# Kernel optimization log

Hardware: AMD Instinct MI355X
Metric: run time of the kernel (lower is better)

The kernel has to match this reference:

```python
import jax, jax.numpy as jnp
import numpy as np

N, F_DIM, H_DIM = 8192, 128, 128

def setup_inputs() -> dict:
    key = jax.random.key(0)
    ks = jax.random.split(key, 7)
    inp = {
        "input": jax.random.normal(ks[0], (N, F_DIM), dtype=jnp.float32),
        "wavelets": jax.random.normal(ks[1], (N, N), dtype=jnp.float32) / np.sqrt(N),
        "wavelets_inv": jax.random.normal(ks[2], (N, N), dtype=jnp.float32) / np.sqrt(N),
        # layer 1 params
        "W1": jax.random.uniform(ks[3], (F_DIM, H_DIM), dtype=jnp.float32,
                                 minval=-np.sqrt(6.0/(F_DIM+H_DIM)), maxval=np.sqrt(6.0/(F_DIM+H_DIM))),
        "f1": jax.random.uniform(ks[4], (N,), dtype=jnp.float32, minval=0.9, maxval=1.1),
        # layer 2 params
        "W2": jax.random.uniform(ks[5], (H_DIM, H_DIM), dtype=jnp.float32,
                                 minval=-np.sqrt(6.0/(H_DIM+H_DIM)), maxval=np.sqrt(6.0/(H_DIM+H_DIM))),
        "f2": jax.random.uniform(ks[6], (N,), dtype=jnp.float32, minval=0.9, maxval=1.1),
    }
    return inp

def _gwnn_layer(features, wavelets, wavelets_inv, W, filt):
    # torch: wavelets @ diag(filt) @ (wavelets_inv @ (features @ W))
    # diag(filt) matmul == column-wise scale of wavelets (broadcast elementwise)
    xw = features @ W                      # [N, out]
    spec = wavelets_inv @ xw               # [N, out] spectral-domain features
    spec = filt[:, None] * spec            # apply learnable diagonal filter
    return wavelets @ spec                 # [N, out]

def reference(input, wavelets, wavelets_inv, W1, f1, W2, f2):
    # eval mode: dropout is identity
    h1 = jax.nn.relu(_gwnn_layer(input, wavelets, wavelets_inv, W1, f1))
    out = _gwnn_layer(h1, wavelets, wavelets_inv, W2, f2)
    return out
```

## Files before the change

### kernel.cpp

```cpp
#include <hip/hip_runtime.h>
#include <hip/hip_bf16.h>
#include <stdint.h>


typedef __attribute__((ext_vector_type(4))) float f32x4;
typedef __attribute__((ext_vector_type(8))) short s16x8;
typedef __attribute__((ext_vector_type(4))) short s16x4;

#define DEVI static __device__ __forceinline__

DEVI short bf1(float x){ __bf16 h = (__bf16)x; return __builtin_bit_cast(short, h); }

DEVI s16x8 cvt8(f32x4 lo, f32x4 hi){
  s16x8 r;
#pragma unroll
  for (int i = 0; i < 4; ++i){ r[i] = bf1(lo[i]); r[4+i] = bf1(hi[i]); }
  return r;
}

DEVI void glds16(const void* g, void* l){
  __builtin_amdgcn_global_load_lds((const __attribute__((address_space(1))) void*)g,
                                   (__attribute__((address_space(3))) void*)l, 16, 0, 0);
}

template<int N> DEVI void waitvm(){
  if constexpr (N == 0)       asm volatile("s_waitcnt vmcnt(0)"  ::: "memory");
  else if constexpr (N == 5)  asm volatile("s_waitcnt vmcnt(5)"  ::: "memory");
  else if constexpr (N == 6)  asm volatile("s_waitcnt vmcnt(6)"  ::: "memory");
  else if constexpr (N == 12) asm volatile("s_waitcnt vmcnt(12)" ::: "memory");
}

__global__ __launch_bounds__(256, 1) void gemm_big(
    const float* __restrict__ Ap, const short* __restrict__ Btp,
    float* __restrict__ Pp, int K, int M)
{
  constexpr int BM = 128, BK = 64;
  constexpr int ASZ = BM*BK*4;
  constexpr int BSZ = 128*BK*2;
  constexpr int TSZ = ASZ + BSZ;
  constexpr int NBUF = 3, PRE = 2;
  __shared__ uint8_t lds[NBUF*TSZ];

  const int tid  = threadIdx.x;
  const int lane = tid & 63;
  const int wv   = tid >> 6;
  const int la   = lane & 15;
  const int g4   = lane >> 4;
  const int bxl  = ((blockIdx.x & 7) << 3) + (blockIdx.x >> 3);
  const int m0   = bxl * BM;
  const int kq   = blockIdx.y;
  const int K4   = K >> 2;
  const int kb   = kq * K4;

  const float* gAbase = Ap + (size_t)m0*K + kb;
  int aoffg[8];
#pragma unroll
  for (int j = 0; j < 8; ++j){
    const int rl = (wv<<5) + (j<<2) + (lane>>4);
    aoffg[j] = rl*K + (((lane&15) ^ (rl&15))<<2);
  }

  const int nb0 = (wv<<5) + (lane>>3);
  const short* gB0 = Btp + (size_t)(nb0    )*K + kb + (((lane&7)^(nb0&7))<<3);
  const short* gB1 = Btp + (size_t)(nb0+ 8 )*K + kb + (((lane&7)^(nb0&7))<<3);
  const short* gB2 = Btp + (size_t)(nb0+16 )*K + kb + (((lane&7)^(nb0&7))<<3);
  const short* gB3 = Btp + (size_t)(nb0+24 )*K + kb + (((lane&7)^(nb0&7))<<3);

  int aoff[2][2][2];
#pragma unroll
  for (int mi = 0; mi < 2; ++mi){
    const int r = (wv<<5) + mi*16 + la;
#pragma unroll
    for (int kf = 0; kf < 2; ++kf){
      const int v0 = kf*8 + (g4<<1);
      aoff[mi][kf][0] = r*256 + (((v0  )^(r&15))<<4);
      aoff[mi][kf][1] = r*256 + (((v0+1)^(r&15))<<4);
    }
  }
  int boff[8][2];
#pragma unroll
  for (int ni = 0; ni < 8; ++ni){
    const int n = ni*16 + la;
#pragma unroll
    for (int kf = 0; kf < 2; ++kf){
      const int u = kf*4 + g4;
      boff[ni][kf] = n*128 + ((u^(n&7))<<4);
    }
  }

  f32x4 acc[2][8] = {};

  int kk = 0;
  uint8_t* const lend = lds + NBUF*TSZ;
  uint8_t* bs = lds;
  uint8_t* bc = lds;

  auto STAGE = [&](){
    uint8_t* Ab = bs;
    uint8_t* Bb = bs + ASZ;
#pragma unroll
    for (int j = 0; j < 8; ++j)
      glds16(gAbase + aoffg[j] + kk, Ab + (wv<<13) + (j<<10));
    kk += BK;
    glds16(gB0, Bb + (wv<<12));
    glds16(gB1, Bb + (wv<<12) + 1024);
    glds16(gB2, Bb + (wv<<12) + 2048);
    glds16(gB3, Bb + (wv<<12) + 3072);
    gB0 += BK; gB1 += BK; gB2 += BK; gB3 += BK;
    bs += TSZ; if (bs == lend) bs = lds;
  };

  auto COMPUTE = [&](){
    const uint8_t* Ab = bc;
    const uint8_t* Bb = bc + ASZ;
#pragma unroll
    for (int kf = 0; kf < 2; ++kf){
      s16x8 a0 = cvt8(*(const f32x4*)(Ab + aoff[0][kf][0]),
                      *(const f32x4*)(Ab + aoff[0][kf][1]));
      s16x8 a1 = cvt8(*(const f32x4*)(Ab + aoff[1][kf][0]),
                      *(const f32x4*)(Ab + aoff[1][kf][1]));
#pragma unroll
      for (int ni = 0; ni < 8; ++ni){
        s16x8 b = *(const s16x8*)(Bb + boff[ni][kf]);
        acc[0][ni] = __builtin_amdgcn_mfma_f32_16x16x32_bf16(a0, b, acc[0][ni], 0, 0, 0);
        acc[1][ni] = __builtin_amdgcn_mfma_f32_16x16x32_bf16(a1, b, acc[1][ni], 0, 0, 0);
      }
    }
    bc += TSZ; if (bc == lend) bc = lds;
  };

  const int ns = K4 >> 6;
  for (int s = 0; s < PRE && s < ns; ++s) STAGE();

  for (int t = 0; t < ns; ++t){
    if (t < ns - 1) waitvm<12>();
    else            waitvm<0>();
    __builtin_amdgcn_s_barrier();
    asm volatile("" ::: "memory");
    if (t + PRE < ns) STAGE();
    COMPUTE();
    asm volatile("" ::: "memory");
  }

  float* P = Pp + (size_t)kq * M * 128;
  const int rbase = m0 + (wv<<5) + (g4<<2);
#pragma unroll
  for (int mi = 0; mi < 2; ++mi)
#pragma unroll
    for (int ni = 0; ni < 8; ++ni)
#pragma unroll
      for (int r = 0; r < 4; ++r)
        P[(size_t)(rbase + mi*16 + r)*128 + ni*16 + la] = acc[mi][ni][r];
}

template<bool ABF>
__global__ __launch_bounds__(256, 1) void sgemm(
    const void* __restrict__ Ap, const short* __restrict__ Btp,
    void* __restrict__ Outp, int K, int M)
{
  constexpr int BM = 32, BN = 128, BK = 64;
  constexpr int ASZ = ABF ? BM*BK*2 : BM*BK*4;
  constexpr int BSZ = BN*BK*2;
  constexpr int TSZ = ASZ + BSZ;
  constexpr int NL  = ABF ? 5 : 6;
  constexpr int NBUF = 3, PRE = 2;
  __shared__ uint8_t lds[NBUF*TSZ];

  const int tid  = threadIdx.x;
  const int lane = tid & 63;
  const int wv   = tid >> 6;
  const int la   = lane & 15;
  const int g4   = lane >> 4;
  const int m0   = blockIdx.x * BM;

  const float* gA0 = nullptr; const float* gA1 = nullptr; const short* gAh = nullptr;
  if constexpr (!ABF){
    const float* Af = (const float*)Ap;
    int r0 = (wv<<3) + (lane>>4);
    int r1 = r0 + 4;
    gA0 = Af + (size_t)(m0+r0)*K + (((lane&15)^(r0&15))<<2);
    gA1 = Af + (size_t)(m0+r1)*K + (((lane&15)^(r1&15))<<2);
  } else {
    const short* Ah = (const short*)Ap;
    int r = (wv<<3) + (lane>>3);
    gAh = Ah + (size_t)(m0+r)*K + (((lane&7)^(r&7))<<3);
  }
  const int nb0 = (wv<<5) + (lane>>3);
  const short* gB0 = Btp + (size_t)(nb0    )*K + (((lane&7)^(nb0&7))<<3);
  const short* gB1 = Btp + (size_t)(nb0+ 8 )*K + (((lane&7)^(nb0&7))<<3);
  const short* gB2 = Btp + (size_t)(nb0+16 )*K + (((lane&7)^(nb0&7))<<3);
  const short* gB3 = Btp + (size_t)(nb0+24 )*K + (((lane&7)^(nb0&7))<<3);

  int aoff[2][2][2];
  int boff[2][2];
#pragma unroll
  for (int mi = 0; mi < 2; ++mi){
    const int r = mi*16 + la;
#pragma unroll
    for (int kf = 0; kf < 2; ++kf){
      if constexpr (!ABF){
        const int v0 = kf*8 + (g4<<1);
        aoff[mi][kf][0] = r*256 + (((v0  )^(r&15))<<4);
        aoff[mi][kf][1] = r*256 + (((v0+1)^(r&15))<<4);
      } else {
        const int u = kf*4 + g4;
        aoff[mi][kf][0] = r*128 + ((u^(r&7))<<4);
        aoff[mi][kf][1] = 0;
      }
    }
  }
#pragma unroll
  for (int ni = 0; ni < 2; ++ni){
    const int n = (wv<<5) + ni*16 + la;
#pragma unroll
    for (int kf = 0; kf < 2; ++kf){
      const int u = kf*4 + g4;
      boff[ni][kf] = n*128 + ((u^(n&7))<<4);
    }
  }

  f32x4 acc[2][2] = {};

  auto STAGE = [&](uint8_t* buf){
    uint8_t* Ab = buf;
    uint8_t* Bb = buf + ASZ;
    if constexpr (!ABF){
      glds16(gA0, Ab + (wv<<11));
      glds16(gA1, Ab + (wv<<11) + 1024);
      gA0 += BK; gA1 += BK;
    } else {
      glds16(gAh, Ab + (wv<<10));
      gAh += BK;
    }
    glds16(gB0, Bb + (wv<<12));
    glds16(gB1, Bb + (wv<<12) + 1024);
    glds16(gB2, Bb + (wv<<12) + 2048);
    glds16(gB3, Bb + (wv<<12) + 3072);
    gB0 += BK; gB1 += BK; gB2 += BK; gB3 += BK;
  };

  auto COMPUTE = [&](const uint8_t* buf){
    const uint8_t* Ab = buf;
    const uint8_t* Bb = buf + ASZ;
#pragma unroll
    for (int kf = 0; kf < 2; ++kf){
      s16x8 a0, a1, b0, b1;
      if constexpr (!ABF){
        a0 = cvt8(*(const f32x4*)(Ab + aoff[0][kf][0]), *(const f32x4*)(Ab + aoff[0][kf][1]));
        a1 = cvt8(*(const f32x4*)(Ab + aoff[1][kf][0]), *(const f32x4*)(Ab + aoff[1][kf][1]));
      } else {
        a0 = *(const s16x8*)(Ab + aoff[0][kf][0]);
        a1 = *(const s16x8*)(Ab + aoff[1][kf][0]);
      }
      b0 = *(const s16x8*)(Bb + boff[0][kf]);
      b1 = *(const s16x8*)(Bb + boff[1][kf]);
      acc[0][0] = __builtin_amdgcn_mfma_f32_16x16x32_bf16(a0, b0, acc[0][0], 0, 0, 0);
      acc[0][1] = __builtin_amdgcn_mfma_f32_16x16x32_bf16(a0, b1, acc[0][1], 0, 0, 0);
      acc[1][0] = __builtin_amdgcn_mfma_f32_16x16x32_bf16(a1, b0, acc[1][0], 0, 0, 0);
      acc[1][1] = __builtin_amdgcn_mfma_f32_16x16x32_bf16(a1, b1, acc[1][1], 0, 0, 0);
    }
  };

  const int ns = K >> 6;
  uint8_t* const lend = lds + NBUF*TSZ;
  uint8_t* bs = lds;
  uint8_t* bc = lds;
  for (int s = 0; s < PRE && s < ns; ++s){
    STAGE(bs);
    bs += TSZ; if (bs == lend) bs = lds;
  }
  for (int t = 0; t < ns; ++t){
    if (t < ns - 1) waitvm<NL>(); else waitvm<0>();
    __builtin_amdgcn_s_barrier();
    asm volatile("" ::: "memory");
    if (t + PRE < ns){
      STAGE(bs);
      bs += TSZ; if (bs == lend) bs = lds;
    }
    COMPUTE(bc);
    bc += TSZ; if (bc == lend) bc = lds;
    asm volatile("" ::: "memory");
  }

  const int mbase = m0 + (g4<<2);
  const int nc0   = (wv<<5) + la;
#pragma unroll
  for (int mi = 0; mi < 2; ++mi){
#pragma unroll
    for (int ni = 0; ni < 2; ++ni){
      s16x4 pk;
#pragma unroll
      for (int r = 0; r < 4; ++r) pk[r] = bf1(acc[mi][ni][r]);
      *(s16x4*)((short*)Outp + (size_t)(nc0 + (ni<<4))*M + (mbase + (mi<<4))) = pk;
    }
  }
}


__global__ __launch_bounds__(256) void red_t(
    const float* __restrict__ Pp, const float* __restrict__ fp,
    short* __restrict__ out, int M)
{
  __shared__ short t[128*65];
  const size_t S = (size_t)M*128;
  const int m0 = blockIdx.x * 64;
  const int tid = threadIdx.x;
#pragma unroll
  for (int it = 0; it < 8; ++it){
    const int idx = it*256 + tid;
    const int m = idx >> 5, nq = idx & 31;
    const float* base = Pp + (size_t)(m0+m)*128;
    f32x4 a = ((const f32x4*)(base      ))[nq];
    f32x4 b = ((const f32x4*)(base +   S))[nq];
    f32x4 c = ((const f32x4*)(base + 2*S))[nq];
    f32x4 d = ((const f32x4*)(base + 3*S))[nq];
    const float fv = fp[m0+m];
#pragma unroll
    for (int j = 0; j < 4; ++j)
      t[(nq*4+j)*65 + m] = bf1(fv * ((a[j] + b[j]) + (c[j] + d[j])));
  }
  __syncthreads();
#pragma unroll
  for (int it = 0; it < 8; ++it){
    const int idx = it*256 + tid;
    const int n = idx >> 4, mc = idx & 15;
    s16x4 v;
#pragma unroll
    for (int j = 0; j < 4; ++j) v[j] = t[n*65 + mc*4 + j];
    *(s16x4*)(out + (size_t)n*M + m0 + mc*4) = v;
  }
}

__global__ __launch_bounds__(256) void red_r(
    const float* __restrict__ Pp, short* __restrict__ out, int M)
{
  const size_t S = (size_t)M*128;
  const size_t i0 = (size_t)(blockIdx.x*256 + threadIdx.x) * 8;
  s16x8 v;
#pragma unroll
  for (int h = 0; h < 2; ++h){
    f32x4 a = *(const f32x4*)(Pp + i0 + 4*h);
    f32x4 b = *(const f32x4*)(Pp + i0 + 4*h + S);
    f32x4 c = *(const f32x4*)(Pp + i0 + 4*h + 2*S);
    f32x4 d = *(const f32x4*)(Pp + i0 + 4*h + 3*S);
#pragma unroll
    for (int j = 0; j < 4; ++j)
      v[4*h+j] = bf1(fmaxf((a[j] + b[j]) + (c[j] + d[j]), 0.0f));
  }
  *(s16x8*)(out + i0) = v;
}

__global__ __launch_bounds__(256) void red_f(
    const float* __restrict__ Pp, float* __restrict__ out, int M)
{
  const size_t S = (size_t)M*128;
  const size_t i0 = (size_t)(blockIdx.x*256 + threadIdx.x) * 4;
  f32x4 a = *(const f32x4*)(Pp + i0);
  f32x4 b = *(const f32x4*)(Pp + i0 + S);
  f32x4 c = *(const f32x4*)(Pp + i0 + 2*S);
  f32x4 d = *(const f32x4*)(Pp + i0 + 3*S);
  *(f32x4*)(out + i0) = (a + b) + (c + d);
}

__global__ void wtrans_k(const float* __restrict__ W1, const float* __restrict__ W2,
                         short* __restrict__ T1, short* __restrict__ T2){
  const int idx = blockIdx.x*256 + threadIdx.x;
  const int m = idx >> 14, rem = idx & 16383;
  const int n = rem >> 7, k = rem & 127;
  const float* W = m ? W2 : W1;
  short* T = m ? T2 : T1;
  T[n*128 + k] = bf1(W[k*128 + n]);
}

extern "C" void kernel_launch(void* const* d_in, const int* in_sizes, int n_in,
                              void* d_out, int out_size, void* d_ws, size_t ws_size,
                              hipStream_t stream){
  const float* input = (const float*)d_in[0];
  const float* wav   = (const float*)d_in[1];
  const float* winv  = (const float*)d_in[2];
  const float* W1    = (const float*)d_in[3];
  const float* f1    = (const float*)d_in[4];
  const float* W2    = (const float*)d_in[5];
  const float* f2    = (const float*)d_in[6];

  constexpr int M = 8192;
  uint8_t* ws = (uint8_t*)d_ws;
  short* W1T = (short*)(ws);
  short* W2T = (short*)(ws + (32<<10));
  short* XWT = (short*)(ws + (64<<10));
  short* SPT = (short*)(ws + (64<<10) + (2<<20));
  short* H1  = (short*)(ws + (64<<10) + (4<<20));
  float* P   = (float*)(ws + (64<<10) + (6<<20));

  dim3 b(256);
  dim3 gbig(M/128, 4);
  dim3 gns(M/32);
  dim3 grt(M/64);
  dim3 grr(M*128/(256*8));
  dim3 grf(M*128/(256*4));
  dim3 gt(128);

  wtrans_k<<<gt, b, 0, stream>>>(W1, W2, W1T, W2T);
  sgemm<false><<<gns, b, 0, stream>>>(input, W1T, XWT, 128, M);
  gemm_big<<<gbig, b, 0, stream>>>(winv, XWT, P, M, M);
  red_t  <<<grt, b, 0, stream>>>(P, f1, SPT, M);
  gemm_big<<<gbig, b, 0, stream>>>(wav, SPT, P, M, M);
  red_r  <<<grr, b, 0, stream>>>(P, H1, M);
  sgemm<true ><<<gns, b, 0, stream>>>(H1, W2T, XWT, 128, M);
  gemm_big<<<gbig, b, 0, stream>>>(winv, XWT, P, M, M);
  red_t  <<<grt, b, 0, stream>>>(P, f2, SPT, M);
  gemm_big<<<gbig, b, 0, stream>>>(wav, SPT, P, M, M);
  red_f  <<<grf, b, 0, stream>>>(P, (float*)d_out, M);
}
```

Measured before the change: 290.2 us.

## Halve K-tile and deepen LDS pipeline to four stages in flight

Shrinks the K tile of the big split-K GEMM from 64 to 32 and raises the ring from 3 to 6 LDS buffers, with 4 stages prefetched instead of 2. The global-to-LDS load mapping, swizzle offsets and vmcnt waits are rewritten to match the smaller tile. The aim is to keep more memory requests in flight to hide latency on this bandwidth-bound fp32-A GEMM. The cost is twice as many barriers per unit of K and less MFMA work between synchronisations.

```diff
diff --git a/kernel.cpp b/kernel.cpp
--- a/kernel.cpp
+++ b/kernel.cpp
@@ -28,17 +28,18 @@
   else if constexpr (N == 5)  asm volatile("s_waitcnt vmcnt(5)"  ::: "memory");
   else if constexpr (N == 6)  asm volatile("s_waitcnt vmcnt(6)"  ::: "memory");
   else if constexpr (N == 12) asm volatile("s_waitcnt vmcnt(12)" ::: "memory");
+  else if constexpr (N == 18) asm volatile("s_waitcnt vmcnt(18)" ::: "memory");
 }
 
 __global__ __launch_bounds__(256, 1) void gemm_big(
     const float* __restrict__ Ap, const short* __restrict__ Btp,
     float* __restrict__ Pp, int K, int M)
 {
-  constexpr int BM = 128, BK = 64;
+  constexpr int BM = 128, BK = 32;
   constexpr int ASZ = BM*BK*4;
   constexpr int BSZ = 128*BK*2;
   constexpr int TSZ = ASZ + BSZ;
-  constexpr int NBUF = 3, PRE = 2;
+  constexpr int NBUF = 6, PRE = 4;
   __shared__ uint8_t lds[NBUF*TSZ];
 
   const int tid  = threadIdx.x;
@@ -53,39 +54,30 @@
   const int kb   = kq * K4;
 
   const float* gAbase = Ap + (size_t)m0*K + kb;
-  int aoffg[8];
-#pragma unroll
-  for (int j = 0; j < 8; ++j){
-    const int rl = (wv<<5) + (j<<2) + (lane>>4);
-    aoffg[j] = rl*K + (((lane&15) ^ (rl&15))<<2);
-  }
-
-  const int nb0 = (wv<<5) + (lane>>3);
-  const short* gB0 = Btp + (size_t)(nb0    )*K + kb + (((lane&7)^(nb0&7))<<3);
-  const short* gB1 = Btp + (size_t)(nb0+ 8 )*K + kb + (((lane&7)^(nb0&7))<<3);
-  const short* gB2 = Btp + (size_t)(nb0+16 )*K + kb + (((lane&7)^(nb0&7))<<3);
-  const short* gB3 = Btp + (size_t)(nb0+24 )*K + kb + (((lane&7)^(nb0&7))<<3);
-
-  int aoff[2][2][2];
+  int aoffg[4];
+#pragma unroll
+  for (int j = 0; j < 4; ++j){
+    const int rl = (wv<<5) + (j<<3) + (lane>>3);
+    aoffg[j] = rl*K + (((lane&7) ^ (rl&7))<<2);
+  }
+
+  const int nb0 = (wv<<5) + (lane>>2);
+  const short* gB0 = Btp + (size_t)(nb0    )*K + kb + (((lane&3)^(nb0&3))<<3);
+  const short* gB1 = Btp + (size_t)(nb0+16 )*K + kb + (((lane&3)^(nb0&3))<<3);
+
+  int aoff[2][2];
 #pragma unroll
   for (int mi = 0; mi < 2; ++mi){
     const int r = (wv<<5) + mi*16 + la;
 #pragma unroll
-    for (int kf = 0; kf < 2; ++kf){
-      const int v0 = kf*8 + (g4<<1);
-      aoff[mi][kf][0] = r*256 + (((v0  )^(r&15))<<4);
-      aoff[mi][kf][1] = r*256 + (((v0+1)^(r&15))<<4);
-    }
-  }
-  int boff[8][2];
+    for (int p = 0; p < 2; ++p)
+      aoff[mi][p] = r*128 + ((((g4<<1)+p)^(r&7))<<4);
+  }
+  int boff[8];
 #pragma unroll
   for (int ni = 0; ni < 8; ++ni){
     const int n = ni*16 + la;
-#pragma unroll
-    for (int kf = 0; kf < 2; ++kf){
-      const int u = kf*4 + g4;
-      boff[ni][kf] = n*128 + ((u^(n&7))<<4);
-    }
+    boff[ni] = n*64 + ((g4^(n&3))<<4);
   }
 
   f32x4 acc[2][8] = {};
@@ -99,42 +91,40 @@
     uint8_t* Ab = bs;
     uint8_t* Bb = bs + ASZ;
 #pragma unroll
-    for (int j = 0; j < 8; ++j)
-      glds16(gAbase + aoffg[j] + kk, Ab + (wv<<13) + (j<<10));
+    for (int j = 0; j < 4; ++j)
+      glds16(gAbase + aoffg[j] + kk, Ab + (wv<<12) + (j<<10));
     kk += BK;
-    glds16(gB0, Bb + (wv<<12));
-    glds16(gB1, Bb + (wv<<12) + 1024);
-    glds16(gB2, Bb + (wv<<12) + 2048);
-    glds16(gB3, Bb + (wv<<12) + 3072);
-    gB0 += BK; gB1 += BK; gB2 += BK; gB3 += BK;
+    glds16(gB0, Bb + (wv<<11));
+    glds16(gB1, Bb + (wv<<11) + 1024);
+    gB0 += BK; gB1 += BK;
     bs += TSZ; if (bs == lend) bs = lds;
   };
 
   auto COMPUTE = [&](){
     const uint8_t* Ab = bc;
     const uint8_t* Bb = bc + ASZ;
-#pragma unroll
-    for (int kf = 0; kf < 2; ++kf){
-      s16x8 a0 = cvt8(*(const f32x4*)(Ab + aoff[0][kf][0]),
-                      *(const f32x4*)(Ab + aoff[0][kf][1]));
-      s16x8 a1 = cvt8(*(const f32x4*)(Ab + aoff[1][kf][0]),
-                      *(const f32x4*)(Ab + aoff[1][kf][1]));
-#pragma unroll
-      for (int ni = 0; ni < 8; ++ni){
-        s16x8 b = *(const s16x8*)(Bb + boff[ni][kf]);
-        acc[0][ni] = __builtin_amdgcn_mfma_f32_16x16x32_bf16(a0, b, acc[0][ni], 0, 0, 0);
-        acc[1][ni] = __builtin_amdgcn_mfma_f32_16x16x32_bf16(a1, b, acc[1][ni], 0, 0, 0);
-      }
+    s16x8 a0 = cvt8(*(const f32x4*)(Ab + aoff[0][0]),
+                    *(const f32x4*)(Ab + aoff[0][1]));
+    s16x8 a1 = cvt8(*(const f32x4*)(Ab + aoff[1][0]),
+                    *(const f32x4*)(Ab + aoff[1][1]));
+#pragma unroll
+    for (int ni = 0; ni < 8; ++ni){
+      s16x8 b = *(const s16x8*)(Bb + boff[ni]);
+      acc[0][ni] = __builtin_amdgcn_mfma_f32_16x16x32_bf16(a0, b, acc[0][ni], 0, 0, 0);
+      acc[1][ni] = __builtin_amdgcn_mfma_f32_16x16x32_bf16(a1, b, acc[1][ni], 0, 0, 0);
     }
     bc += TSZ; if (bc == lend) bc = lds;
   };
 
-  const int ns = K4 >> 6;
+  const int ns = K4 >> 5;
   for (int s = 0; s < PRE && s < ns; ++s) STAGE();
 
   for (int t = 0; t < ns; ++t){
-    if (t < ns - 1) waitvm<12>();
-    else            waitvm<0>();
+    const int ahead = ns - 1 - t;
+    if (ahead >= 3)      waitvm<18>();
+    else if (ahead == 2) waitvm<12>();
+    else if (ahead == 1) waitvm<6>();
+    else                 waitvm<0>();
     __builtin_amdgcn_s_barrier();
     asm volatile("" ::: "memory");
     if (t + PRE < ns) STAGE();
```

Result: slower. 299.2 us (+3.1%).

## Fuse split-K reductions into big GEMM via last-block atomic counter

Applied to the files above, without the earlier changes.

Removes the separate split-K reduction kernels (red_t, red_r, red_f). Each gemm_big block now writes its partial tile, bumps an atomic counter per M-tile, and the fourth-arriving block sums the four partials and applies the filter/transpose, ReLU, or plain store. This cuts four launches and their launch gaps, at the cost of a serialized reduction tail in the last block of each tile. It also needs a memset of the counters on every call.

```diff
diff --git a/kernel.cpp b/kernel.cpp
--- a/kernel.cpp
+++ b/kernel.cpp
@@ -30,9 +30,11 @@
   else if constexpr (N == 12) asm volatile("s_waitcnt vmcnt(12)" ::: "memory");
 }
 
+template<int OUTM>
 __global__ __launch_bounds__(256, 1) void gemm_big(
     const float* __restrict__ Ap, const short* __restrict__ Btp,
-    float* __restrict__ Pp, int K, int M)
+    float* __restrict__ Pp, unsigned int* __restrict__ cnt,
+    const float* __restrict__ fp, void* __restrict__ Outp, int K, int M)
 {
   constexpr int BM = 128, BK = 64;
   constexpr int ASZ = BM*BK*4;
@@ -40,6 +42,7 @@
   constexpr int TSZ = ASZ + BSZ;
   constexpr int NBUF = 3, PRE = 2;
   __shared__ uint8_t lds[NBUF*TSZ];
+  __shared__ int lastf;
 
   const int tid  = threadIdx.x;
   const int lane = tid & 63;
@@ -142,15 +145,71 @@
     asm volatile("" ::: "memory");
   }
 
-  float* P = Pp + (size_t)kq * M * 128;
-  const int rbase = m0 + (wv<<5) + (g4<<2);
-#pragma unroll
-  for (int mi = 0; mi < 2; ++mi)
-#pragma unroll
-    for (int ni = 0; ni < 8; ++ni)
-#pragma unroll
-      for (int r = 0; r < 4; ++r)
-        P[(size_t)(rbase + mi*16 + r)*128 + ni*16 + la] = acc[mi][ni][r];
+  {
+    float* P = Pp + (size_t)kq * M * 128;
+    const int rbase = m0 + (wv<<5) + (g4<<2);
+#pragma unroll
+    for (int mi = 0; mi < 2; ++mi)
+#pragma unroll
+      for (int ni = 0; ni < 8; ++ni)
+#pragma unroll
+        for (int r = 0; r < 4; ++r)
+          P[(size_t)(rbase + mi*16 + r)*128 + ni*16 + la] = acc[mi][ni][r];
+  }
+
+  __threadfence();
+  __syncthreads();
+  if (tid == 0){
+    unsigned int old = atomicAdd(&cnt[bxl], 1u);
+    lastf = (old == 3u);
+  }
+  __syncthreads();
+  if (!lastf) return;
+  __threadfence();
+
+  const size_t S = (size_t)M * 128;
+  const float* Pb = Pp + (size_t)m0 * 128;
+
+  if constexpr (OUTM == 1 || OUTM == 0){
+#pragma unroll
+    for (int it = 0; it < 16; ++it){
+      const int idx = it*256 + tid;
+      const int row = idx >> 5, c = idx & 31;
+      const float* p = Pb + (size_t)row*128 + c*4;
+      f32x4 v = (*(const f32x4*)(p) + *(const f32x4*)(p + S))
+              + (*(const f32x4*)(p + 2*S) + *(const f32x4*)(p + 3*S));
+      if constexpr (OUTM == 1){
+        s16x4 pk;
+#pragma unroll
+        for (int j = 0; j < 4; ++j) pk[j] = bf1(fmaxf(v[j], 0.0f));
+        *(s16x4*)((short*)Outp + (size_t)(m0 + row)*128 + c*4) = pk;
+      } else {
+        *(f32x4*)((float*)Outp + (size_t)(m0 + row)*128 + c*4) = v;
+      }
+    }
+  } else {
+    short* T = (short*)lds;
+#pragma unroll
+    for (int it = 0; it < 16; ++it){
+      const int idx = it*256 + tid;
+      const int row = idx >> 5, c = idx & 31;
+      const float* p = Pb + (size_t)row*128 + c*4;
+      f32x4 v = (*(const f32x4*)(p) + *(const f32x4*)(p + S))
+              + (*(const f32x4*)(p + 2*S) + *(const f32x4*)(p + 3*S));
+      const float fv = fp[m0 + row];
+#pragma unroll
+      for (int j = 0; j < 4; ++j)
+        T[(c*4 + j)*132 + row] = bf1(fv * v[j]);
+    }
+    __syncthreads();
+#pragma unroll
+    for (int it = 0; it < 16; ++it){
+      const int idx = it*256 + tid;
+      const int n = idx >> 5, c = idx & 31;
+      s16x4 val = *(const s16x4*)(T + n*132 + c*4);
+      *(s16x4*)((short*)Outp + (size_t)n*M + m0 + c*4) = val;
+    }
+  }
 }
 
 template<bool ABF>
@@ -296,72 +355,6 @@
   }
 }
 
-
-__global__ __launch_bounds__(256) void red_t(
-    const float* __restrict__ Pp, const float* __restrict__ fp,
-    short* __restrict__ out, int M)
-{
-  __shared__ short t[128*65];
-  const size_t S = (size_t)M*128;
-  const int m0 = blockIdx.x * 64;
-  const int tid = threadIdx.x;
-#pragma unroll
-  for (int it = 0; it < 8; ++it){
-    const int idx = it*256 + tid;
-    const int m = idx >> 5, nq = idx & 31;
-    const float* base = Pp + (size_t)(m0+m)*128;
-    f32x4 a = ((const f32x4*)(base      ))[nq];
-    f32x4 b = ((const f32x4*)(base +   S))[nq];
-    f32x4 c = ((const f32x4*)(base + 2*S))[nq];
-    f32x4 d = ((const f32x4*)(base + 3*S))[nq];
-    const float fv = fp[m0+m];
-#pragma unroll
-    for (int j = 0; j < 4; ++j)
-      t[(nq*4+j)*65 + m] = bf1(fv * ((a[j] + b[j]) + (c[j] + d[j])));
-  }
-  __syncthreads();
-#pragma unroll
-  for (int it = 0; it < 8; ++it){
-    const int idx = it*256 + tid;
-    const int n = idx >> 4, mc = idx & 15;
-    s16x4 v;
-#pragma unroll
-    for (int j = 0; j < 4; ++j) v[j] = t[n*65 + mc*4 + j];
-    *(s16x4*)(out + (size_t)n*M + m0 + mc*4) = v;
-  }
-}
-
-__global__ __launch_bounds__(256) void red_r(
-    const float* __restrict__ Pp, short* __restrict__ out, int M)
-{
-  const size_t S = (size_t)M*128;
-  const size_t i0 = (size_t)(blockIdx.x*256 + threadIdx.x) * 8;
-  s16x8 v;
-#pragma unroll
-  for (int h = 0; h < 2; ++h){
-    f32x4 a = *(const f32x4*)(Pp + i0 + 4*h);
-    f32x4 b = *(const f32x4*)(Pp + i0 + 4*h + S);
-    f32x4 c = *(const f32x4*)(Pp + i0 + 4*h + 2*S);
-    f32x4 d = *(const f32x4*)(Pp + i0 + 4*h + 3*S);
-#pragma unroll
-    for (int j = 0; j < 4; ++j)
-      v[4*h+j] = bf1(fmaxf((a[j] + b[j]) + (c[j] + d[j]), 0.0f));
-  }
-  *(s16x8*)(out + i0) = v;
-}
-
-__global__ __launch_bounds__(256) void red_f(
-    const float* __restrict__ Pp, float* __restrict__ out, int M)
-{
-  const size_t S = (size_t)M*128;
-  const size_t i0 = (size_t)(blockIdx.x*256 + threadIdx.x) * 4;
-  f32x4 a = *(const f32x4*)(Pp + i0);
-  f32x4 b = *(const f32x4*)(Pp + i0 + S);
-  f32x4 c = *(const f32x4*)(Pp + i0 + 2*S);
-  f32x4 d = *(const f32x4*)(Pp + i0 + 3*S);
-  *(f32x4*)(out + i0) = (a + b) + (c + d);
-}
-
 __global__ void wtrans_k(const float* __restrict__ W1, const float* __restrict__ W2,
                          short* __restrict__ T1, short* __restrict__ T2){
   const int idx = blockIdx.x*256 + threadIdx.x;
@@ -390,25 +383,20 @@
   short* XWT = (short*)(ws + (64<<10));
   short* SPT = (short*)(ws + (64<<10) + (2<<20));
   short* H1  = (short*)(ws + (64<<10) + (4<<20));
-  float* P   = (float*)(ws + (64<<10) + (6<<20));
+  unsigned int* CNT = (unsigned int*)(ws + (64<<10) + (6<<20));
+  float* P   = (float*)(ws + (64<<10) + (6<<20) + (4<<10));
 
   dim3 b(256);
   dim3 gbig(M/128, 4);
   dim3 gns(M/32);
-  dim3 grt(M/64);
-  dim3 grr(M*128/(256*8));
-  dim3 grf(M*128/(256*4));
   dim3 gt(128);
 
+  hipMemsetAsync(CNT, 0, 4*64*sizeof(unsigned int), stream);
   wtrans_k<<<gt, b, 0, stream>>>(W1, W2, W1T, W2T);
   sgemm<false><<<gns, b, 0, stream>>>(input, W1T, XWT, 128, M);
-  gemm_big<<<gbig, b, 0, stream>>>(winv, XWT, P, M, M);
-  red_t  <<<grt, b, 0, stream>>>(P, f1, SPT, M);
-  gemm_big<<<gbig, b, 0, stream>>>(wav, SPT, P, M, M);
-  red_r  <<<grr, b, 0, stream>>>(P, H1, M);
+  gemm_big<2><<<gbig, b, 0, stream>>>(winv, XWT, P, CNT      , f1, SPT, M, M);
+  gemm_big<1><<<gbig, b, 0, stream>>>(wav,  SPT, P, CNT +  64, nullptr, H1, M, M);
   sgemm<true ><<<gns, b, 0, stream>>>(H1, W2T, XWT, 128, M);
-  gemm_big<<<gbig, b, 0, stream>>>(winv, XWT, P, M, M);
-  red_t  <<<grt, b, 0, stream>>>(P, f2, SPT, M);
-  gemm_big<<<gbig, b, 0, stream>>>(wav, SPT, P, M, M);
-  red_f  <<<grf, b, 0, stream>>>(P, (float*)d_out, M);
-}
+  gemm_big<2><<<gbig, b, 0, stream>>>(winv, XWT, P, CNT + 128, f2, SPT, M, M);
+  gemm_big<0><<<gbig, b, 0, stream>>>(wav,  SPT, P, CNT + 192, nullptr, d_out, M, M);
+}
```

New measurement: 423.8 us. +46.1%, slower.

## Halve big GEMM row tile and double-buffer to fit two blocks per CU

Applied to the files above, without the earlier changes.

Shrinks the big fp32-A GEMM tile from 128 to 64 rows, which doubles the grid and halves accumulators and A staging. It switches from a triple-buffered prefetch-2 pipeline to a double-buffered prefetch-1 pipeline with an extra barrier per iteration, and sets launch bounds to allow two blocks per CU. The aim is more resident waves and more blocks to hide memory latency on this memory-bound GEMM. In exchange, each B tile is reused over fewer rows, so B traffic doubles, and the extra barrier adds synchronisation cost.

```diff
diff --git a/kernel.cpp b/kernel.cpp
--- a/kernel.cpp
+++ b/kernel.cpp
@@ -24,21 +24,21 @@
 }
 
 template<int N> DEVI void waitvm(){
-  if constexpr (N == 0)       asm volatile("s_waitcnt vmcnt(0)"  ::: "memory");
-  else if constexpr (N == 5)  asm volatile("s_waitcnt vmcnt(5)"  ::: "memory");
-  else if constexpr (N == 6)  asm volatile("s_waitcnt vmcnt(6)"  ::: "memory");
-  else if constexpr (N == 12) asm volatile("s_waitcnt vmcnt(12)" ::: "memory");
-}
-
-__global__ __launch_bounds__(256, 1) void gemm_big(
+  if constexpr (N == 0)      asm volatile("s_waitcnt vmcnt(0)" ::: "memory");
+  else if constexpr (N == 5) asm volatile("s_waitcnt vmcnt(5)" ::: "memory");
+  else if constexpr (N == 6) asm volatile("s_waitcnt vmcnt(6)" ::: "memory");
+  else if constexpr (N == 8) asm volatile("s_waitcnt vmcnt(8)" ::: "memory");
+}
+
+__global__ __launch_bounds__(256, 2) void gemm_big(
     const float* __restrict__ Ap, const short* __restrict__ Btp,
     float* __restrict__ Pp, int K, int M)
 {
-  constexpr int BM = 128, BK = 64;
+  constexpr int BM = 64, BK = 64;
   constexpr int ASZ = BM*BK*4;
   constexpr int BSZ = 128*BK*2;
   constexpr int TSZ = ASZ + BSZ;
-  constexpr int NBUF = 3, PRE = 2;
+  constexpr int NBUF = 2;
   __shared__ uint8_t lds[NBUF*TSZ];
 
   const int tid  = threadIdx.x;
@@ -46,17 +46,17 @@
   const int wv   = tid >> 6;
   const int la   = lane & 15;
   const int g4   = lane >> 4;
-  const int bxl  = ((blockIdx.x & 7) << 3) + (blockIdx.x >> 3);
+  const int bxl  = ((blockIdx.x & 7) << 4) + (blockIdx.x >> 3);
   const int m0   = bxl * BM;
   const int kq   = blockIdx.y;
   const int K4   = K >> 2;
   const int kb   = kq * K4;
 
   const float* gAbase = Ap + (size_t)m0*K + kb;
-  int aoffg[8];
-#pragma unroll
-  for (int j = 0; j < 8; ++j){
-    const int rl = (wv<<5) + (j<<2) + (lane>>4);
+  int aoffg[4];
+#pragma unroll
+  for (int j = 0; j < 4; ++j){
+    const int rl = (wv<<4) + (j<<2) + (lane>>4);
     aoffg[j] = rl*K + (((lane&15) ^ (rl&15))<<2);
   }
 
@@ -66,15 +66,14 @@
   const short* gB2 = Btp + (size_t)(nb0+16 )*K + kb + (((lane&7)^(nb0&7))<<3);
   const short* gB3 = Btp + (size_t)(nb0+24 )*K + kb + (((lane&7)^(nb0&7))<<3);
 
-  int aoff[2][2][2];
-#pragma unroll
-  for (int mi = 0; mi < 2; ++mi){
-    const int r = (wv<<5) + mi*16 + la;
+  int aoff[2][2];
+  {
+    const int r = (wv<<4) + la;
 #pragma unroll
     for (int kf = 0; kf < 2; ++kf){
       const int v0 = kf*8 + (g4<<1);
-      aoff[mi][kf][0] = r*256 + (((v0  )^(r&15))<<4);
-      aoff[mi][kf][1] = r*256 + (((v0+1)^(r&15))<<4);
+      aoff[kf][0] = r*256 + (((v0  )^(r&15))<<4);
+      aoff[kf][1] = r*256 + (((v0+1)^(r&15))<<4);
     }
   }
   int boff[8][2];
@@ -88,7 +87,7 @@
     }
   }
 
-  f32x4 acc[2][8] = {};
+  f32x4 acc[8] = {};
 
   int kk = 0;
   uint8_t* const lend = lds + NBUF*TSZ;
@@ -99,8 +98,8 @@
     uint8_t* Ab = bs;
     uint8_t* Bb = bs + ASZ;
 #pragma unroll
-    for (int j = 0; j < 8; ++j)
-      glds16(gAbase + aoffg[j] + kk, Ab + (wv<<13) + (j<<10));
+    for (int j = 0; j < 4; ++j)
+      glds16(gAbase + aoffg[j] + kk, Ab + (wv<<12) + (j<<10));
     kk += BK;
     glds16(gB0, Bb + (wv<<12));
     glds16(gB1, Bb + (wv<<12) + 1024);
@@ -115,42 +114,37 @@
     const uint8_t* Bb = bc + ASZ;
 #pragma unroll
     for (int kf = 0; kf < 2; ++kf){
-      s16x8 a0 = cvt8(*(const f32x4*)(Ab + aoff[0][kf][0]),
-                      *(const f32x4*)(Ab + aoff[0][kf][1]));
-      s16x8 a1 = cvt8(*(const f32x4*)(Ab + aoff[1][kf][0]),
-                      *(const f32x4*)(Ab + aoff[1][kf][1]));
+      s16x8 a = cvt8(*(const f32x4*)(Ab + aoff[kf][0]),
+                     *(const f32x4*)(Ab + aoff[kf][1]));
 #pragma unroll
       for (int ni = 0; ni < 8; ++ni){
         s16x8 b = *(const s16x8*)(Bb + boff[ni][kf]);
-        acc[0][ni] = __builtin_amdgcn_mfma_f32_16x16x32_bf16(a0, b, acc[0][ni], 0, 0, 0);
-        acc[1][ni] = __builtin_amdgcn_mfma_f32_16x16x32_bf16(a1, b, acc[1][ni], 0, 0, 0);
+        acc[ni] = __builtin_amdgcn_mfma_f32_16x16x32_bf16(a, b, acc[ni], 0, 0, 0);
       }
     }
     bc += TSZ; if (bc == lend) bc = lds;
   };
 
   const int ns = K4 >> 6;
-  for (int s = 0; s < PRE && s < ns; ++s) STAGE();
+  STAGE();
 
   for (int t = 0; t < ns; ++t){
-    if (t < ns - 1) waitvm<12>();
-    else            waitvm<0>();
+    if (t + 1 < ns){ STAGE(); waitvm<8>(); }
+    else           { waitvm<0>(); }
     __builtin_amdgcn_s_barrier();
     asm volatile("" ::: "memory");
-    if (t + PRE < ns) STAGE();
     COMPUTE();
     asm volatile("" ::: "memory");
+    __builtin_amdgcn_s_barrier();
   }
 
   float* P = Pp + (size_t)kq * M * 128;
-  const int rbase = m0 + (wv<<5) + (g4<<2);
-#pragma unroll
-  for (int mi = 0; mi < 2; ++mi)
-#pragma unroll
-    for (int ni = 0; ni < 8; ++ni)
-#pragma unroll
-      for (int r = 0; r < 4; ++r)
-        P[(size_t)(rbase + mi*16 + r)*128 + ni*16 + la] = acc[mi][ni][r];
+  const int rbase = m0 + (wv<<4) + (g4<<2);
+#pragma unroll
+  for (int ni = 0; ni < 8; ++ni)
+#pragma unroll
+    for (int r = 0; r < 4; ++r)
+      P[(size_t)(rbase + r)*128 + ni*16 + la] = acc[ni][r];
 }
 
 template<bool ABF>
@@ -393,7 +387,7 @@
   float* P   = (float*)(ws + (64<<10) + (6<<20));
 
   dim3 b(256);
-  dim3 gbig(M/128, 4);
+  dim3 gbig(M/64, 4);
   dim3 gns(M/32);
   dim3 grt(M/64);
   dim3 grr(M*128/(256*8));
```

New measurement: 322.2 us. 11.1% more time.
